# Kernel tuning notes

Measured on AMD Instinct MI355X. Metric: run time of the kernel, lower is better.

## Reference

```python
import jax, jax.numpy as jnp
import numpy as np
from jax import lax

V_TH = 1.0    # base firing threshold
RHO = 0.9     # adaptive-threshold decay
ADAPT = 0.1   # threshold increment per spike
SLOPE = 5.0   # surrogate-gradient sigmoid slope

@jax.custom_vjp
def spike_fn(v):
    return (v >= 0.0).astype(v.dtype)

def _spike_fwd(v):
    return spike_fn(v), v

def _spike_bwd(v, g):
    s = jax.nn.sigmoid(SLOPE * v)
    return (g * SLOPE * s * (1.0 - s),)

spike_fn.defvjp(_spike_fwd, _spike_bwd)

def lif_scan(x_seq, beta):
    # x_seq: (T, ..., F) channel-last; beta: (F,). Adaptive LIF with soft reset.
    def step(carry, x):
        mem, b = carry
        mem = beta * mem + x
        th = V_TH + b
        spk = spike_fn(mem - th)
        mem = mem - spk * th
        b = RHO * b + ADAPT * spk
        return (mem, b), spk
    z = jnp.zeros_like(x_seq[0])
    _, spikes = lax.scan(step, (z, z), x_seq)
    return spikes

def conv2d_s2(x, w, b):
    # NCHW conv, stride 2, padding 1
    y = lax.conv_general_dilated(x, w, (2, 2), ((1, 1), (1, 1)),
                                 dimension_numbers=('NCHW', 'OIHW', 'NCHW'))
    return y + b[None, :, None, None]

def mha(x, wq, wk, wv, wo, nh=4):
    B, T, D = x.shape
    dh = D // nh
    q = (x @ wq.T).reshape(B, T, nh, dh)
    k = (x @ wk.T).reshape(B, T, nh, dh)
    v = (x @ wv.T).reshape(B, T, nh, dh)
    att = jnp.einsum('bqhd,bkhd->bhqk', q, k) * (dh ** -0.5)
    p = jax.nn.softmax(att, axis=-1)
    o = jnp.einsum('bhqk,bkhd->bqhd', p, v).reshape(B, T, D)
    return o @ wo.T

def _forward(x, conv1_w, conv1_b, conv2_w, conv2_b, beta1, beta2,
             proj_w, proj_b, wq, wk, wv, wo, cls_w, cls_b):
    B, T, C, H, W = x.shape
    H1, W1, H2, W2 = H // 2, W // 2, H // 4, W // 4
    # stage 1 conv over all timesteps at once (conv is stateless)
    c1 = conv2d_s2(x.reshape(B * T, C, H, W), conv1_w, conv1_b)       # (B*T,16,H1,W1)
    c1 = jnp.moveaxis(c1.reshape(B, T, 16, H1, W1), 2, -1)            # (B,T,H1,W1,16)
    c1 = jnp.moveaxis(c1, 1, 0)                                       # (T,B,H1,W1,16)
    s1 = lif_scan(c1, beta1)                                          # (T,B,H1,W1,16)
    s1 = jnp.moveaxis(jnp.moveaxis(s1, 0, 1), -1, 2)                  # (B,T,16,H1,W1)
    # stage 2
    c2 = conv2d_s2(s1.reshape(B * T, 16, H1, W1), conv2_w, conv2_b)   # (B*T,32,H2,W2)
    c2 = jnp.moveaxis(c2.reshape(B, T, 32, H2, W2), 2, -1)
    c2 = jnp.moveaxis(c2, 1, 0)                                       # (T,B,H2,W2,32)
    s2 = lif_scan(c2, beta2)                                          # (T,B,H2,W2,32)
    total_spikes = s2.sum()
    # flatten channel-major to match torch permute(0,3,1,2).view(B,-1)
    feats = jnp.moveaxis(s2, -1, 2)                                   # (T,B,32,H2,W2)
    feats = jnp.moveaxis(feats, 0, 1).reshape(B, T, -1)               # (B,T,32*H2*W2)
    proj = feats @ proj_w.T + proj_b                                  # (B,T,64)
    attn = mha(proj, wq, wk, wv, wo)                                  # (B,T,64)
    context = attn.mean(axis=1)                                       # (B,64)
    # lif_out single step from zero state: mem = context
    spk_out = spike_fn(context - V_TH)
    logits = spk_out @ cls_w.T + cls_b
    sparsity = 1.0 - total_spikes / float(feats.size)
    return logits, sparsity

def setup_inputs() -> dict:
    key = jax.random.key(0)
    ks = jax.random.split(key, 10)
    B, T, C, H, W = 64, 8, 2, 128, 128
    D = 64
    flat = 32 * (H // 4) * (W // 4)  # 32768
    f = jnp.float32
    return {
        'x': (jax.random.uniform(ks[0], (B, T, C, H, W)) < 0.1).astype(f),  # sparse DVS events
        'conv1_w': jax.random.normal(ks[1], (16, C, 3, 3), f) * 0.2,
        'conv1_b': jnp.zeros((16,), f),
        'conv2_w': jax.random.normal(ks[2], (32, 16, 3, 3), f) * 0.1,
        'conv2_b': jnp.zeros((32,), f),
        'beta1': jnp.full((16,), 0.9, f),
        'beta2': jnp.full((32,), 0.9, f),
        'proj_w': jax.random.normal(ks[3], (D, flat), f) * (flat ** -0.5),
        'proj_b': jnp.zeros((D,), f),
        'wq': jax.random.normal(ks[4], (D, D), f) * (D ** -0.5),
        'wk': jax.random.normal(ks[5], (D, D), f) * (D ** -0.5),
        'wv': jax.random.normal(ks[6], (D, D), f) * (D ** -0.5),
        'wo': jax.random.normal(ks[7], (D, D), f) * (D ** -0.5),
        'cls_w': jax.random.normal(ks[8], (2, D), f) * (D ** -0.5),
        'cls_b': jnp.zeros((2,), f),
    }

def reference(x, conv1_w, conv1_b, conv2_w, conv2_b, beta1, beta2,
              proj_w, proj_b, wq, wk, wv, wo, cls_w, cls_b):
    return _forward(x, conv1_w, conv1_b, conv2_w, conv2_b, beta1, beta2,
                    proj_w, proj_b, wq, wk, wv, wo, cls_w, cls_b)
```

## Files before the change

### kernel.cpp

```cpp
#include <hip/hip_runtime.h>
#include <cstdint>

#define V_TH 1.0f
#define RHO 0.9f
#define ADAPT 0.1f

static constexpr int B = 64, T = 8, C = 2, H = 128, W = 128;
static constexpr int H1 = 64, W1 = 64;
static constexpr int H2 = 32, W2 = 32;
static constexpr int FLAT = 32 * H2 * W2;
static constexpr int R = B * T;

static constexpr size_t OFF_TRIP  = 0;
static constexpr size_t OFF_BITS  = OFF_TRIP + 8388608;
static constexpr size_t OFF_PWT   = OFF_BITS + 2097152;
static constexpr size_t OFF_CNT   = OFF_PWT + 8388608;
static constexpr size_t OFF_TBL   = OFF_CNT + 256;
static constexpr size_t OFF_PART  = OFF_TBL + 6291456;

__global__ __launch_bounds__(256) void k_mega1(
    const float* __restrict__ x, const float* __restrict__ w,
    const float* __restrict__ bias, const float* __restrict__ beta,
    uint64_t* __restrict__ trip,
    const float* __restrict__ pw, float* __restrict__ pwt,
    const float* __restrict__ c2w, float* __restrict__ tbl,
    unsigned int* __restrict__ cnt) {
  __shared__ float shmem[64 * 65];
  int bid = blockIdx.x;
  int tid = threadIdx.x;
  if (bid < 1024) {
    float* sw1 = shmem;
    for (int i = tid; i < 288; i += 256) {
      int c = i / 18, j = i % 18;
      sw1[j * 68 + c] = w[i];
    }
    __syncthreads();
    int gid = bid * 256 + tid;
    int w1 = gid & 63, h1 = (gid >> 6) & 63, b = gid >> 12;
    int lane = tid & 63;
    float bias_r[16], beta_r[16];
#pragma unroll
    for (int c = 0; c < 16; ++c) { bias_r[c] = bias[c]; beta_r[c] = beta[c]; }
    float mem[16], bth[16];
#pragma unroll
    for (int c = 0; c < 16; ++c) { mem[c] = 0.f; bth[c] = 0.f; }
    for (int t = 0; t < T; ++t) {
      int r = b * T + t;
      const float* xb = x + (size_t)(r * 2) * 16384;
      uint32_t M = 0;
#pragma unroll
      for (int ci = 0; ci < 2; ++ci) {
#pragma unroll
        for (int kh = 0; kh < 3; ++kh) {
          int y = 2 * h1 - 1 + kh;
          uint32_t w3 = 0;
          if (y >= 0 && y < H) {
            float2 v = *(const float2*)(xb + ci * 16384 + y * 128 + 2 * lane);
            float nl = __shfl(v.y, lane - 1, 64);
            uint32_t bl = (lane > 0 && nl != 0.f) ? 1u : 0u;
            uint32_t bm = (v.x != 0.f) ? 2u : 0u;
            uint32_t br = (v.y != 0.f) ? 4u : 0u;
            w3 = bl | bm | br;
          }
          M |= w3 << ((ci * 3 + kh) * 3);
        }
      }
      float acc[16];
#pragma unroll
      for (int c = 0; c < 16; ++c) acc[c] = bias_r[c];
      while (M) {
        int j = __ffs(M) - 1; M &= M - 1;
        const float4* wr = (const float4*)&sw1[j * 68];
        float4 a0 = wr[0], a1 = wr[1], a2 = wr[2], a3 = wr[3];
        acc[0] += a0.x; acc[1] += a0.y; acc[2] += a0.z; acc[3] += a0.w;
        acc[4] += a1.x; acc[5] += a1.y; acc[6] += a1.z; acc[7] += a1.w;
        acc[8] += a2.x; acc[9] += a2.y; acc[10] += a2.z; acc[11] += a2.w;
        acc[12] += a3.x; acc[13] += a3.y; acc[14] += a3.z; acc[15] += a3.w;
      }
      uint32_t mask = 0;
#pragma unroll
      for (int c = 0; c < 16; ++c) {
        mem[c] = beta_r[c] * mem[c] + acc[c];
        float th = V_TH + bth[c];
        bool s = (mem[c] >= th);
        if (s) { mem[c] -= th; mask |= (1u << c); }
        bth[c] = RHO * bth[c] + (s ? ADAPT : 0.f);
      }
      int iL = 2 * lane - 1; if (iL < 0) iL = 0;
      uint32_t mL = __shfl((int)mask, iL, 64);
      uint32_t mC = __shfl((int)mask, 2 * lane, 64);
      uint32_t mR = __shfl((int)mask, 2 * lane + 1, 64);
      if (lane < 32) {
        uint64_t tw = (uint64_t)(lane ? mL : 0u) | ((uint64_t)mC << 16) |
                      ((uint64_t)mR << 32);
        trip[(size_t)(r * H1 + h1) * 32 + lane] = tw;
      }
    }
  } else if (bid < 1536) {
    float* tile = shmem;
    int tb = bid - 1024;
    int c = tb >> 4, pt = tb & 15;
    int posc = ((c & 3) << 3) + (c >> 2);
    int p0 = pt * 64;
    int lane = tid & 63, quad = tid >> 6;
#pragma unroll
    for (int it = 0; it < 16; ++it) {
      int d = it * 4 + quad;
      tile[d * 65 + lane] = pw[(size_t)d * FLAT + c * 1024 + p0 + lane];
    }
    __syncthreads();
#pragma unroll
    for (int it = 0; it < 16; ++it) {
      int pp = it * 4 + quad;
      pwt[((size_t)((p0 + pp) * 32 + posc)) * 64 + lane] = tile[lane * 65 + pp];
    }
  } else if (bid == 1536) {
    if (tid == 0) *cnt = 0u;
  } else {
    int idx = bid - 1537;
    int g = idx >> 4;
    int kh = g >> 2, gp = g & 3;
    int v = ((idx & 15) << 8) + tid;
    float e[32];
#pragma unroll
    for (int co = 0; co < 32; ++co) e[co] = 0.f;
    for (int i = 0; i < 12; ++i) {
      if ((v >> i) & 1) {
        int j = gp * 12 + i;
        int kw = j >> 4, ci = j & 15;
#pragma unroll
        for (int co = 0; co < 32; ++co)
          e[co] += c2w[((co * 16 + ci) * 3 + kh) * 3 + kw];
      }
    }
#pragma unroll
    for (int co = 0; co < 32; ++co)
      tbl[((size_t)(g * 4096 + v)) * 32 + co] = e[co];
  }
}

__global__ __launch_bounds__(256) void k_conv2_lif2(
    const uint64_t* __restrict__ trip, const float* __restrict__ tbl,
    const float* __restrict__ bias, const float* __restrict__ beta,
    uint32_t* __restrict__ bits, unsigned int* __restrict__ cnt) {
  __shared__ unsigned int sc;
  int tid = threadIdx.x;
  if (tid == 0) sc = 0u;
  __syncthreads();
  int lane = tid & 63;
  int li = lane & 7;
  int p8 = lane >> 3;
  int wvi = (blockIdx.x * 256 + tid) >> 6;
  int px = wvi * 8 + p8;
  int w2 = px & 31, h2 = (px >> 5) & 31, b = px >> 10;
  float4 b4 = *(const float4*)&bias[4 * li];
  float4 bt4 = *(const float4*)&beta[4 * li];
  float m0v = 0.f, m1v = 0.f, m2v = 0.f, m3v = 0.f;
  float t0 = 0.f, t1 = 0.f, t2 = 0.f, t3 = 0.f;
  unsigned int lc = 0;
  const float4* tb4 = (const float4*)tbl;
  for (int t = 0; t < T; ++t) {
    int r = b * T + t;
    const uint64_t* tr = trip + (size_t)(r * 64 + 2 * h2) * 32 + w2;
    uint64_t q0 = (h2 > 0) ? tr[-32] : 0ull;
    uint64_t q1 = tr[0];
    uint64_t q2 = tr[32];
    uint32_t r0l = (uint32_t)q0, r0h = (uint32_t)(q0 >> 32);
    uint32_t r1l = (uint32_t)q1, r1h = (uint32_t)(q1 >> 32);
    uint32_t r2l = (uint32_t)q2, r2h = (uint32_t)(q2 >> 32);
    float4 v0 = tb4[(0 << 15) + ((r0l & 4095u) << 3) + li];
    float4 v1 = tb4[(1 << 15) + (((r0l >> 12) & 4095u) << 3) + li];
    float4 v2 = tb4[(2 << 15) + ((((r0l >> 24) | (r0h << 8)) & 4095u) << 3) + li];
    float4 v3 = tb4[(3 << 15) + (((r0h >> 4) & 4095u) << 3) + li];
    float4 v4 = tb4[(4 << 15) + ((r1l & 4095u) << 3) + li];
    float4 v5 = tb4[(5 << 15) + (((r1l >> 12) & 4095u) << 3) + li];
    float4 v6 = tb4[(6 << 15) + ((((r1l >> 24) | (r1h << 8)) & 4095u) << 3) + li];
    float4 v7 = tb4[(7 << 15) + (((r1h >> 4) & 4095u) << 3) + li];
    float4 v8 = tb4[(8 << 15) + ((r2l & 4095u) << 3) + li];
    float4 v9 = tb4[(9 << 15) + (((r2l >> 12) & 4095u) << 3) + li];
    float4 va = tb4[(10 << 15) + ((((r2l >> 24) | (r2h << 8)) & 4095u) << 3) + li];
    float4 vb = tb4[(11 << 15) + (((r2h >> 4) & 4095u) << 3) + li];
    float A0 = b4.x + v0.x + v1.x + v2.x + v3.x;
    float A1 = b4.y + v0.y + v1.y + v2.y + v3.y;
    float A2 = b4.z + v0.z + v1.z + v2.z + v3.z;
    float A3 = b4.w + v0.w + v1.w + v2.w + v3.w;
    float B0 = v4.x + v5.x + v6.x + v7.x;
    float B1 = v4.y + v5.y + v6.y + v7.y;
    float B2 = v4.z + v5.z + v6.z + v7.z;
    float B3 = v4.w + v5.w + v6.w + v7.w;
    float C0 = v8.x + v9.x + va.x + vb.x;
    float C1 = v8.y + v9.y + va.y + vb.y;
    float C2 = v8.z + v9.z + va.z + vb.z;
    float C3 = v8.w + v9.w + va.w + vb.w;
    float a0 = (A0 + B0) + C0, a1 = (A1 + B1) + C1;
    float a2 = (A2 + B2) + C2, a3 = (A3 + B3) + C3;
    m0v = bt4.x * m0v + a0;
    m1v = bt4.y * m1v + a1;
    m2v = bt4.z * m2v + a2;
    m3v = bt4.w * m3v + a3;
    float th0 = V_TH + t0, th1 = V_TH + t1, th2 = V_TH + t2, th3 = V_TH + t3;
    bool s0 = (m0v >= th0), s1 = (m1v >= th1), s2 = (m2v >= th2), s3 = (m3v >= th3);
    if (s0) m0v -= th0;
    if (s1) m1v -= th1;
    if (s2) m2v -= th2;
    if (s3) m3v -= th3;
    t0 = RHO * t0 + (s0 ? ADAPT : 0.f);
    t1 = RHO * t1 + (s1 ? ADAPT : 0.f);
    t2 = RHO * t2 + (s2 ? ADAPT : 0.f);
    t3 = RHO * t3 + (s3 ? ADAPT : 0.f);
    unsigned long long bl0 = __ballot(s0);
    unsigned long long bl1 = __ballot(s1);
    unsigned long long bl2 = __ballot(s2);
    unsigned long long bl3 = __ballot(s3);
    if (li == 0) {
      int sh = p8 * 8;
      uint32_t m32 = ((uint32_t)(bl0 >> sh) & 0xFFu)
                   | (((uint32_t)(bl1 >> sh) & 0xFFu) << 8)
                   | (((uint32_t)(bl2 >> sh) & 0xFFu) << 16)
                   | (((uint32_t)(bl3 >> sh) & 0xFFu) << 24);
      bits[(size_t)r * 1024 + (px & 1023)] = m32;
      lc += __popc(m32);
    }
  }
  if (li == 0) atomicAdd(&sc, lc);
  __syncthreads();
  if (tid == 0) atomicAdd(cnt, sc);
}

__global__ __launch_bounds__(256) void k_proj_gemm(
    const uint32_t* __restrict__ bits, const float* __restrict__ pwt,
    float* __restrict__ partial) {
  int rt = blockIdx.x >> 4;
  int ks = (blockIdx.x & 15) * 4 + (threadIdx.x >> 6);
  int d = threadIdx.x & 63;
  float acc[8] = {0, 0, 0, 0, 0, 0, 0, 0};
  const uint32_t* bb = bits + (size_t)rt * 8 * 1024;
  for (int wi = 0; wi < 16; ++wi) {
    int word = ks * 16 + wi;
    const float* rowbase = pwt + ((size_t)word * 32) * 64 + d;
#pragma unroll
    for (int ri = 0; ri < 8; ++ri) {
      uint32_t m = bb[ri * 1024 + word];
      while (m) {
        int c = __ffs(m) - 1; m &= m - 1;
        acc[ri] += rowbase[c << 6];
      }
    }
  }
#pragma unroll
  for (int ri = 0; ri < 8; ++ri)
    partial[((size_t)(rt * 64 + ks) * 8 + ri) * 64 + d] = acc[ri];
}

__global__ __launch_bounds__(256) void k_attn_final(
    const float* __restrict__ partial, const float* __restrict__ pb,
    const float* __restrict__ wq, const float* __restrict__ wk,
    const float* __restrict__ wv, const float* __restrict__ wo,
    const float* __restrict__ clsw, const float* __restrict__ clsb,
    const unsigned int* __restrict__ cnt, float* __restrict__ out) {
  __shared__ float swq[64 * 65], swk[64 * 65], swv[64 * 65], swo[64 * 65];
  __shared__ float sp[8 * 65], sq[8 * 65], sk[8 * 65], sv[8 * 65], so2[8 * 65];
  __shared__ float satt[4][8][8];
  __shared__ float sob[64];
  int b = blockIdx.x, tid = threadIdx.x;
  for (int i = tid; i < 4096; i += 256) {
    int dd = i >> 6, e = i & 63;
    swq[dd * 65 + e] = wq[i]; swk[dd * 65 + e] = wk[i];
    swv[dd * 65 + e] = wv[i]; swo[dd * 65 + e] = wo[i];
  }
  for (int i = tid; i < 512; i += 256) {
    int ri = i >> 6, d = i & 63;
    float s = pb[d];
    const float* p = partial + ((size_t)(b * 64) * 8 + ri) * 64 + d;
#pragma unroll
    for (int ks = 0; ks < 64; ++ks) s += p[(size_t)ks * 512];
    sp[ri * 65 + d] = s;
  }
  __syncthreads();
#pragma unroll
  for (int p = 0; p < 2; ++p) {
    int idx = p * 256 + tid, t = idx >> 6, d = idx & 63;
    float qa = 0.f, ka = 0.f, va = 0.f;
    for (int e = 0; e < 64; ++e) {
      float pe = sp[t * 65 + e];
      qa += pe * swq[d * 65 + e];
      ka += pe * swk[d * 65 + e];
      va += pe * swv[d * 65 + e];
    }
    sq[t * 65 + d] = qa; sk[t * 65 + d] = ka; sv[t * 65 + d] = va;
  }
  __syncthreads();
  {
    int h = tid >> 6, q = (tid >> 3) & 7, k = tid & 7;
    float s = 0.f;
    for (int j = 0; j < 16; ++j)
      s += sq[q * 65 + h * 16 + j] * sk[k * 65 + h * 16 + j];
    satt[h][q][k] = s * 0.25f;
  }
  __syncthreads();
  if (tid < 32) {
    int h = tid >> 3, q2 = tid & 7;
    float m = -1e30f;
    for (int k2 = 0; k2 < 8; ++k2) m = fmaxf(m, satt[h][q2][k2]);
    float sum = 0.f;
    for (int k2 = 0; k2 < 8; ++k2) {
      float e = expf(satt[h][q2][k2] - m);
      satt[h][q2][k2] = e; sum += e;
    }
    float inv = 1.f / sum;
    for (int k2 = 0; k2 < 8; ++k2) satt[h][q2][k2] *= inv;
  }
  __syncthreads();
#pragma unroll
  for (int p = 0; p < 2; ++p) {
    int idx = p * 256 + tid, t = idx >> 6, d = idx & 63;
    int h = d >> 4;
    float o = 0.f;
    for (int k = 0; k < 8; ++k) o += satt[h][t][k] * sv[k * 65 + d];
    so2[t * 65 + d] = o;
  }
  __syncthreads();
  if (tid < 64) {
    float ob = 0.f;
    for (int t = 0; t < 8; ++t) ob += so2[t * 65 + tid];
    sob[tid] = ob * 0.125f;
  }
  __syncthreads();
  if (tid < 64) {
    float ctx = 0.f;
    for (int e = 0; e < 64; ++e) ctx += sob[e] * swo[tid * 65 + e];
    int spk = (ctx >= V_TH) ? 1 : 0;
    unsigned long long ball = __ballot(spk);
    if (tid < 2) {
      float lg = clsb[tid];
      for (int dd = 0; dd < 64; ++dd)
        if ((ball >> dd) & 1ull) lg += clsw[tid * 64 + dd];
      out[b * 2 + tid] = lg;
    }
    if (b == 0 && tid == 2)
      out[128] = 1.f - (float)(*cnt) / 16777216.f;
  }
}

extern "C" void kernel_launch(void* const* d_in, const int* in_sizes, int n_in,
                              void* d_out, int out_size, void* d_ws, size_t ws_size,
                              hipStream_t stream) {
  const float* x    = (const float*)d_in[0];
  const float* c1w  = (const float*)d_in[1];
  const float* c1b  = (const float*)d_in[2];
  const float* c2w  = (const float*)d_in[3];
  const float* c2b  = (const float*)d_in[4];
  const float* bt1  = (const float*)d_in[5];
  const float* bt2  = (const float*)d_in[6];
  const float* pw   = (const float*)d_in[7];
  const float* pb   = (const float*)d_in[8];
  const float* wq   = (const float*)d_in[9];
  const float* wk   = (const float*)d_in[10];
  const float* wv   = (const float*)d_in[11];
  const float* wo   = (const float*)d_in[12];
  const float* clsw = (const float*)d_in[13];
  const float* clsb = (const float*)d_in[14];
  float* out = (float*)d_out;

  uint8_t* ws = (uint8_t*)d_ws;
  uint64_t* trip  = (uint64_t*)(ws + OFF_TRIP);
  uint32_t* bits  = (uint32_t*)(ws + OFF_BITS);
  float*    pwt   = (float*)(ws + OFF_PWT);
  unsigned int* cnt = (unsigned int*)(ws + OFF_CNT);
  float*    tbl   = (float*)(ws + OFF_TBL);
  float*    part  = (float*)(ws + OFF_PART);

  k_mega1<<<1729, 256, 0, stream>>>(x, c1w, c1b, bt1, trip, pw, pwt, c2w, tbl, cnt);
  k_conv2_lif2<<<2048, 256, 0, stream>>>(trip, tbl, c2b, bt2, bits, cnt);
  k_proj_gemm<<<1024, 256, 0, stream>>>(bits, pwt, part);
  k_attn_final<<<64, 256, 0, stream>>>(part, pb, wq, wk, wv, wo, clsw, clsb, cnt, out);
}
```

Measured before the change: 212.7 us.

## Replace per-bit conv1 accumulation with per-row lookup tables and prefetch next timestep

The first conv stage now builds, per block, a table in shared memory of precomputed weight sums for every 6-bit pattern (3 columns by 2 input channels) of each kernel row. Each output then needs three table lookups instead of a data-dependent loop over set bits. Input rows for the next timestep are also loaded one iteration ahead, to hide global-load latency. The cost is extra table-building work and a shared-memory barrier per block, plus more registers for the prefetched values.

```diff
diff --git a/kernel.cpp b/kernel.cpp
--- a/kernel.cpp
+++ b/kernel.cpp
@@ -25,57 +25,100 @@
     const float* __restrict__ pw, float* __restrict__ pwt,
     const float* __restrict__ c2w, float* __restrict__ tbl,
     unsigned int* __restrict__ cnt) {
-  __shared__ float shmem[64 * 65];
+  __shared__ __align__(16) float shmem[64 * 65];
   int bid = blockIdx.x;
   int tid = threadIdx.x;
   if (bid < 1024) {
-    float* sw1 = shmem;
-    for (int i = tid; i < 288; i += 256) {
-      int c = i / 18, j = i % 18;
-      sw1[j * 68 + c] = w[i];
-    }
+    float4* tb = (float4*)shmem;
+    float* sww = shmem + 3072;
+    for (int i = tid; i < 288; i += 256) sww[i] = w[i];
     __syncthreads();
+    if (tid < 192) {
+      int kh = tid >> 6, v = tid & 63;
+      float e[16];
+#pragma unroll
+      for (int c = 0; c < 16; ++c) e[c] = 0.f;
+#pragma unroll
+      for (int bbit = 0; bbit < 6; ++bbit) {
+        if ((v >> bbit) & 1) {
+          int ci = (bbit >= 3) ? 1 : 0;
+          int kw = bbit - ci * 3;
+          int base = ci * 9 + kh * 3 + kw;
+#pragma unroll
+          for (int c = 0; c < 16; ++c) e[c] += sww[c * 18 + base];
+        }
+      }
+#pragma unroll
+      for (int s = 0; s < 4; ++s)
+        tb[(kh * 4 + s) * 64 + v] =
+            make_float4(e[4 * s], e[4 * s + 1], e[4 * s + 2], e[4 * s + 3]);
+    }
+    __syncthreads();
+
     int gid = bid * 256 + tid;
     int w1 = gid & 63, h1 = (gid >> 6) & 63, b = gid >> 12;
     int lane = tid & 63;
+    (void)w1;
     float bias_r[16], beta_r[16];
 #pragma unroll
     for (int c = 0; c < 16; ++c) { bias_r[c] = bias[c]; beta_r[c] = beta[c]; }
     float mem[16], bth[16];
 #pragma unroll
     for (int c = 0; c < 16; ++c) { mem[c] = 0.f; bth[c] = 0.f; }
+
+    int y0 = 2 * h1 - 1;
+    bool vtop = (y0 >= 0);
+    const float* xb = x + (size_t)(b * T) * 2 * 16384 + 2 * lane;
+
+    float2 cur[6];
+#pragma unroll
+    for (int ci = 0; ci < 2; ++ci)
+#pragma unroll
+      for (int kh = 0; kh < 3; ++kh) {
+        int j = ci * 3 + kh;
+        cur[j] = (kh == 0 && !vtop) ? make_float2(0.f, 0.f)
+               : *(const float2*)(xb + ci * 16384 + (y0 + kh) * 128);
+      }
+
     for (int t = 0; t < T; ++t) {
       int r = b * T + t;
-      const float* xb = x + (size_t)(r * 2) * 16384;
-      uint32_t M = 0;
-#pragma unroll
-      for (int ci = 0; ci < 2; ++ci) {
-#pragma unroll
-        for (int kh = 0; kh < 3; ++kh) {
-          int y = 2 * h1 - 1 + kh;
-          uint32_t w3 = 0;
-          if (y >= 0 && y < H) {
-            float2 v = *(const float2*)(xb + ci * 16384 + y * 128 + 2 * lane);
-            float nl = __shfl(v.y, lane - 1, 64);
-            uint32_t bl = (lane > 0 && nl != 0.f) ? 1u : 0u;
-            uint32_t bm = (v.x != 0.f) ? 2u : 0u;
-            uint32_t br = (v.y != 0.f) ? 4u : 0u;
-            w3 = bl | bm | br;
+      float2 nxt[6];
+      if (t + 1 < T) {
+        const float* xn = xb + (size_t)(t + 1) * 32768;
+#pragma unroll
+        for (int ci = 0; ci < 2; ++ci)
+#pragma unroll
+          for (int kh = 0; kh < 3; ++kh) {
+            int j = ci * 3 + kh;
+            nxt[j] = (kh == 0 && !vtop) ? make_float2(0.f, 0.f)
+                   : *(const float2*)(xn + ci * 16384 + (y0 + kh) * 128);
           }
-          M |= w3 << ((ci * 3 + kh) * 3);
-        }
-      }
+      }
+      uint32_t Mc = 0, Rr = 0;
+#pragma unroll
+      for (int j = 0; j < 6; ++j) {
+        uint32_t bm = (cur[j].x != 0.f) ? 1u : 0u;
+        uint32_t br = (cur[j].y != 0.f) ? 1u : 0u;
+        Mc |= ((bm << 1) | (br << 2)) << (3 * j);
+        Rr |= br << j;
+      }
+      uint32_t RL = (uint32_t)__shfl((int)Rr, lane - 1, 64);
+      if (lane == 0) RL = 0u;
+      uint32_t M = Mc | (RL & 1u) | ((RL & 2u) << 2) | ((RL & 4u) << 4)
+                 | ((RL & 8u) << 6) | ((RL & 16u) << 8) | ((RL & 32u) << 10);
+      int i0 = (int)((M & 7u)         | (((M >> 9) & 7u) << 3));
+      int i1 = (int)(((M >> 3) & 7u)  | (((M >> 12) & 7u) << 3));
+      int i2 = (int)(((M >> 6) & 7u)  | (((M >> 15) & 7u) << 3));
       float acc[16];
 #pragma unroll
-      for (int c = 0; c < 16; ++c) acc[c] = bias_r[c];
-      while (M) {
-        int j = __ffs(M) - 1; M &= M - 1;
-        const float4* wr = (const float4*)&sw1[j * 68];
-        float4 a0 = wr[0], a1 = wr[1], a2 = wr[2], a3 = wr[3];
-        acc[0] += a0.x; acc[1] += a0.y; acc[2] += a0.z; acc[3] += a0.w;
-        acc[4] += a1.x; acc[5] += a1.y; acc[6] += a1.z; acc[7] += a1.w;
-        acc[8] += a2.x; acc[9] += a2.y; acc[10] += a2.z; acc[11] += a2.w;
-        acc[12] += a3.x; acc[13] += a3.y; acc[14] += a3.z; acc[15] += a3.w;
+      for (int s = 0; s < 4; ++s) {
+        float4 u0 = tb[s * 64 + i0];
+        float4 u1 = tb[(4 + s) * 64 + i1];
+        float4 u2 = tb[(8 + s) * 64 + i2];
+        acc[4 * s + 0] = bias_r[4 * s + 0] + u0.x + u1.x + u2.x;
+        acc[4 * s + 1] = bias_r[4 * s + 1] + u0.y + u1.y + u2.y;
+        acc[4 * s + 2] = bias_r[4 * s + 2] + u0.z + u1.z + u2.z;
+        acc[4 * s + 3] = bias_r[4 * s + 3] + u0.w + u1.w + u2.w;
       }
       uint32_t mask = 0;
 #pragma unroll
@@ -94,6 +137,10 @@
         uint64_t tw = (uint64_t)(lane ? mL : 0u) | ((uint64_t)mC << 16) |
                       ((uint64_t)mR << 32);
         trip[(size_t)(r * H1 + h1) * 32 + lane] = tw;
+      }
+      if (t + 1 < T) {
+#pragma unroll
+        for (int j = 0; j < 6; ++j) cur[j] = nxt[j];
       }
     }
   } else if (bid < 1536) {
```

New measurement: 206.2 us. 3.0% less time.
